# Optimization experiments

Measured on AMD Instinct MI355X. Metric: run time of the kernel, lower is better.

The kernel has to match this reference:

```python
import jax, jax.numpy as jnp
import numpy as np

B, S, D, H, W = 8, 2048, 128, 8, 64
INT_HEADS = 8          # hardcoded in SpatioTemporalLayer1
EPS_COS = 1e-8
EPS_LN = 1e-5


def _mha(q_in, k_in, v_in, in_w, in_b, out_w, out_b, nh, mask=None):
    # q_in/k_in/v_in: (batch, len, d); torch nn.MultiheadAttention math (eval, no dropout)
    b, lq, d = q_in.shape
    hd = d // nh
    q = (q_in @ in_w[:d].T + in_b[:d]).reshape(b, lq, nh, hd)
    k = (k_in @ in_w[d:2 * d].T + in_b[d:2 * d]).reshape(b, k_in.shape[1], nh, hd)
    v = (v_in @ in_w[2 * d:].T + in_b[2 * d:]).reshape(b, v_in.shape[1], nh, hd)
    scores = jnp.einsum('bihd,bjhd->bhij', q, k) / jnp.sqrt(jnp.asarray(hd, q_in.dtype))
    if mask is not None:
        scores = scores + mask
    attn = jax.nn.softmax(scores, axis=-1)
    out = jnp.einsum('bhij,bjhd->bihd', attn, v).reshape(b, lq, d)
    return out @ out_w.T + out_b


def _layernorm(x, g, b):
    mu = x.mean(-1, keepdims=True)
    var = ((x - mu) ** 2).mean(-1, keepdims=True)
    return (x - mu) * jax.lax.rsqrt(var + EPS_LN) * g + b


def _cos_normalize(e):
    n = jnp.maximum(jnp.linalg.norm(e, axis=-1, keepdims=True), EPS_COS)
    return e / n


def _forward(x, spatial_info, temporal_info,
             lw_in_w, lw_in_b, lw_out_w, lw_out_b,
             spat_w, spat_b, temp_w, temp_b,
             int_in_w, int_in_b, int_out_w, int_out_b,
             ffn_w1, ffn_b1, ffn_w2, ffn_b2,
             ln1_g, ln1_b, ln2_g, ln2_b):
    b, s, d = x.shape
    # --- local window attention (S % W == 0 here, so no padding path) ---
    nw = s // W
    xw = x.reshape(b * nw, W, d)
    causal = jnp.triu(jnp.full((W, W), -jnp.inf, x.dtype), k=1)
    attn = _mha(xw, xw, xw, lw_in_w, lw_in_b, lw_out_w, lw_out_b, H, causal).reshape(b, s, d)
    x = _layernorm(attn + x, ln1_g, ln1_b)
    # --- FFN (torch nn.GELU default = exact erf) ---
    h = jax.nn.gelu(x @ ffn_w1.T + ffn_b1, approximate=False)
    x = _layernorm(h @ ffn_w2.T + ffn_b2 + x, ln2_g, ln2_b)
    # --- spatio-temporal interaction ---
    se = spatial_info @ spat_w.T + spat_b
    te = temporal_info @ temp_w.T + temp_b
    sn = _cos_normalize(se)
    tn = _cos_normalize(te)
    ss = jnp.einsum('bid,bjd->bij', sn, sn)   # (B,S,S) spatial cosine sim
    ts = jnp.einsum('bid,bjd->bij', tn, tn)   # (B,S,S) temporal cosine sim
    # interaction MHA is batch_first=False: it treats (B,S,D) as (len=B, batch=S, d).
    # Equivalent batch-first call on swapped axes (faithful to the torch source).
    inter = jnp.swapaxes(
        _mha(jnp.swapaxes(se, 0, 1), jnp.swapaxes(te, 0, 1), jnp.swapaxes(te, 0, 1),
             int_in_w, int_in_b, int_out_w, int_out_b, INT_HEADS), 0, 1)
    # similarity[b,i,j,d] = ss[b,i,j]*ts[b,i,j]*inter[b,i,d]; mean over j factorizes:
    sim = (ss * ts).mean(axis=2)              # (B,S)
    return x + sim[..., None] * inter


def setup_inputs() -> dict:
    key = jax.random.key(0)
    ks = jax.random.split(key, 24)
    sc = 0.02
    inp = {
        'x': jax.random.normal(ks[0], (B, S, D), jnp.float32),
        'spatial_info': jax.random.normal(ks[1], (B, S, D), jnp.float32),
        'temporal_info': jax.random.normal(ks[2], (B, S, D), jnp.float32),
        'lw_in_w': jax.random.normal(ks[3], (3 * D, D), jnp.float32) * sc,
        'lw_in_b': jnp.zeros((3 * D,), jnp.float32),
        'lw_out_w': jax.random.normal(ks[4], (D, D), jnp.float32) * sc,
        'lw_out_b': jnp.zeros((D,), jnp.float32),
        'spat_w': jax.random.normal(ks[5], (D, D), jnp.float32) * sc,
        'spat_b': jnp.zeros((D,), jnp.float32),
        'temp_w': jax.random.normal(ks[6], (D, D), jnp.float32) * sc,
        'temp_b': jnp.zeros((D,), jnp.float32),
        'int_in_w': jax.random.normal(ks[7], (3 * D, D), jnp.float32) * sc,
        'int_in_b': jnp.zeros((3 * D,), jnp.float32),
        'int_out_w': jax.random.normal(ks[8], (D, D), jnp.float32) * sc,
        'int_out_b': jnp.zeros((D,), jnp.float32),
        'ffn_w1': jax.random.normal(ks[9], (4 * D, D), jnp.float32) * sc,
        'ffn_b1': jnp.zeros((4 * D,), jnp.float32),
        'ffn_w2': jax.random.normal(ks[10], (D, 4 * D), jnp.float32) * sc,
        'ffn_b2': jnp.zeros((D,), jnp.float32),
        'ln1_g': jnp.ones((D,), jnp.float32),
        'ln1_b': jnp.zeros((D,), jnp.float32),
        'ln2_g': jnp.ones((D,), jnp.float32),
        'ln2_b': jnp.zeros((D,), jnp.float32),
    }
    return inp


def reference(x, spatial_info, temporal_info,
              lw_in_w, lw_in_b, lw_out_w, lw_out_b,
              spat_w, spat_b, temp_w, temp_b,
              int_in_w, int_in_b, int_out_w, int_out_b,
              ffn_w1, ffn_b1, ffn_w2, ffn_b2,
              ln1_g, ln1_b, ln2_g, ln2_b):
    return _forward(x, spatial_info, temporal_info,
                    lw_in_w, lw_in_b, lw_out_w, lw_out_b,
                    spat_w, spat_b, temp_w, temp_b,
                    int_in_w, int_in_b, int_out_w, int_out_b,
                    ffn_w1, ffn_b1, ffn_w2, ffn_b2,
                    ln1_g, ln1_b, ln2_g, ln2_b)
```

## Files before the change

### kernel.cpp

```cpp
#include <hip/hip_runtime.h>
#include <math.h>

#define BB 8
#define SS 2048
#define NTOK (BB * SS)

using bf16x8 = __attribute__((ext_vector_type(8))) short;
using f32x4  = __attribute__((ext_vector_type(4))) float;

__device__ __forceinline__ float gelu_tanh(float x) {
    float y = 0.7978845608f * (x + 0.044715f * x * x * x);
    float e = __expf(2.0f * y);
    float t = 1.0f - 2.0f / (e + 1.0f);
    return 0.5f * x * (1.0f + t);
}
__device__ __forceinline__ unsigned short f2b(float f) {
    unsigned int u = __float_as_uint(f);
    u += 0x7FFFu + ((u >> 16) & 1u);
    return (unsigned short)(u >> 16);
}
__device__ __forceinline__ float b2f(unsigned short u) {
    return __uint_as_float((unsigned int)u << 16);
}
__device__ __forceinline__ bf16x8 ldg_f32_b8(const float* p) {
    float4 f0 = *(const float4*)p, f1 = *(const float4*)(p + 4);
    union { ushort4 u[2]; bf16x8 v; } r;
    r.u[0] = (ushort4){f2b(f0.x), f2b(f0.y), f2b(f0.z), f2b(f0.w)};
    r.u[1] = (ushort4){f2b(f1.x), f2b(f1.y), f2b(f1.z), f2b(f1.w)};
    return r.v;
}

__global__ __launch_bounds__(256) void phase1(
    const float* __restrict__ x,
    const float* __restrict__ lw_in_w, const float* __restrict__ b_in,
    const float* __restrict__ lw_out_w, const float* __restrict__ b_out,
    const float* __restrict__ lng, const float* __restrict__ lnb,
    float* __restrict__ x1, unsigned short* __restrict__ x1b,
    const float* __restrict__ ffn_w1, const float* __restrict__ ffn_w2,
    unsigned short* __restrict__ Wb,
    const float* __restrict__ int_in_w, const float* __restrict__ int_out_w,
    unsigned short* __restrict__ Wib, unsigned short* __restrict__ Wiob,
    float* __restrict__ Mf,
    const float* __restrict__ spatial, const float* __restrict__ temporal,
    const float* __restrict__ spat_w, const float* __restrict__ temp_w,
    const float* __restrict__ bsp, const float* __restrict__ btp,
    unsigned short* __restrict__ snb, unsigned short* __restrict__ tnb,
    unsigned short* __restrict__ seb, unsigned short* __restrict__ teb)
{
    __shared__ unsigned short Qs[64 * 136];
    __shared__ unsigned short Ks[64 * 136];
    __shared__ unsigned short Vt[128 * 72];
    __shared__ unsigned short Pb[4][32 * 72];
    __shared__ float red[2][64][2];
    const int tid = threadIdx.x;
    const int wv = tid >> 6, lane = tid & 63, ln = lane & 15, q = lane >> 4;

    if (blockIdx.x >= 320) {
        const int idx2 = blockIdx.x - 320;
        const int y = idx2 >> 8;
        const int m0 = (idx2 & 255) * 64;
        const float* Af = y ? temporal : spatial;
        const float* Wf = y ? temp_w : spat_w;
        const float* bias = y ? btp : bsp;
        unsigned short* nb = y ? tnb : snb;
        unsigned short* raw = y ? teb : seb;
        const int wm = (wv >> 1) * 32, wn = (wv & 1) * 64;

        f32x4 acc[2][4] = {};
        #pragma unroll
        for (int kf = 0; kf < 4; ++kf) {
            bf16x8 a[2], b[4];
            #pragma unroll
            for (int fm = 0; fm < 2; ++fm)
                a[fm] = ldg_f32_b8(Af + (size_t)(m0 + wm + fm * 16 + ln) * 128 + kf * 32 + q * 8);
            #pragma unroll
            for (int fn = 0; fn < 4; ++fn)
                b[fn] = ldg_f32_b8(Wf + (size_t)(wn + fn * 16 + ln) * 128 + kf * 32 + q * 8);
            #pragma unroll
            for (int fm = 0; fm < 2; ++fm)
                #pragma unroll
                for (int fn = 0; fn < 4; ++fn)
                    acc[fm][fn] = __builtin_amdgcn_mfma_f32_16x16x32_bf16(a[fm], b[fn], acc[fm][fn], 0, 0, 0);
        }
        #pragma unroll
        for (int fm = 0; fm < 2; ++fm)
            #pragma unroll
            for (int r = 0; r < 4; ++r) {
                int rl = wm + fm * 16 + q * 4 + r;
                float s2 = 0.0f;
                #pragma unroll
                for (int fn = 0; fn < 4; ++fn) {
                    int col = wn + fn * 16 + ln;
                    float vv = acc[fm][fn][r] + bias[col];
                    acc[fm][fn][r] = vv;
                    s2 += vv * vv;
                }
                #pragma unroll
                for (int off = 1; off < 16; off <<= 1) s2 += __shfl_xor(s2, off, 64);
                if (ln == 0) red[0][rl][wv & 1] = s2;
            }
        __syncthreads();
        #pragma unroll
        for (int fm = 0; fm < 2; ++fm)
            #pragma unroll
            for (int r = 0; r < 4; ++r) {
                int rl = wm + fm * 16 + q * 4 + r;
                int row = m0 + rl;
                float inv = 1.0f / fmaxf(sqrtf(red[0][rl][0] + red[0][rl][1]), 1e-8f);
                #pragma unroll
                for (int fn = 0; fn < 4; ++fn) {
                    int col = wn + fn * 16 + ln;
                    float vv = acc[fm][fn][r];
                    nb[(size_t)row * 128 + col] = f2b(vv * inv);
                    raw[(size_t)row * 128 + col] = f2b(vv);
                }
            }
        return;
    }

    if (blockIdx.x >= 256) {
        int gt = (blockIdx.x - 256) * 256 + tid;
        #pragma unroll
        for (int s = 0; s < 3; ++s) {
            int v = gt + s * 16384;
            const float* src;
            unsigned short* dst;
            int off;
            if (v < 16384)      { src = ffn_w1;   dst = Wb;         off = v; }
            else if (v < 32768) { src = ffn_w2;   dst = Wb + 65536; off = v - 16384; }
            else if (v < 45056) { src = int_in_w; dst = Wib;        off = v - 32768; }
            else                { src = int_out_w; dst = Wiob;      off = v - 45056; }
            float4 f = *(const float4*)(src + (size_t)off * 4);
            *(ushort4*)(dst + (size_t)off * 4) =
                (ushort4){f2b(f.x), f2b(f.y), f2b(f.z), f2b(f.w)};
        }
        float4 z4 = (float4){0.f, 0.f, 0.f, 0.f};
        *(float4*)(Mf + (size_t)gt * 4) = z4;
        *(float4*)(Mf + (size_t)(gt + 16384) * 4) = z4;
        return;
    }

    const int m0 = blockIdx.x * 64;
    const int wm = (wv >> 1) * 32, wn = (wv & 1) * 64;

    bf16x8 afr[4][2];
    #pragma unroll
    for (int kf = 0; kf < 4; ++kf)
        #pragma unroll
        for (int fm = 0; fm < 2; ++fm)
            afr[kf][fm] = ldg_f32_b8(x + (size_t)(m0 + wm + fm * 16 + ln) * 128 + kf * 32 + q * 8);

    #pragma unroll
    for (int p = 0; p < 3; ++p) {
        f32x4 acc[2][4] = {};
        #pragma unroll
        for (int kf = 0; kf < 4; ++kf) {
            bf16x8 b[4];
            #pragma unroll
            for (int fn = 0; fn < 4; ++fn)
                b[fn] = ldg_f32_b8(lw_in_w + (size_t)(p * 128 + wn + fn * 16 + ln) * 128 + kf * 32 + q * 8);
            #pragma unroll
            for (int fm = 0; fm < 2; ++fm)
                #pragma unroll
                for (int fn = 0; fn < 4; ++fn)
                    acc[fm][fn] = __builtin_amdgcn_mfma_f32_16x16x32_bf16(afr[kf][fm], b[fn], acc[fm][fn], 0, 0, 0);
        }
        #pragma unroll
        for (int fm = 0; fm < 2; ++fm)
            #pragma unroll
            for (int r = 0; r < 4; ++r) {
                int rl = wm + fm * 16 + q * 4 + r;
                #pragma unroll
                for (int fn = 0; fn < 4; ++fn) {
                    int col = wn + fn * 16 + ln;
                    unsigned short v = f2b(acc[fm][fn][r] + b_in[p * 128 + col]);
                    if (p == 0)      Qs[rl * 136 + col] = v;
                    else if (p == 1) Ks[rl * 136 + col] = v;
                    else             Vt[col * 72 + rl] = v;
                }
            }
    }
    __syncthreads();

    {
        const int mh = wv >> 1, hq = wv & 1;
        unsigned short* P = &Pb[wv][0];
        #pragma unroll
        for (int hh = 0; hh < 4; ++hh) {
            const int h = hq * 4 + hh;
            f32x4 sacc[2][4] = {};
            bf16x8 az[2] = {}, bz[4] = {};
            if (q < 2) {
                #pragma unroll
                for (int fm = 0; fm < 2; ++fm)
                    az[fm] = *(const bf16x8*)&Qs[(mh * 32 + fm * 16 + ln) * 136 + h * 16 + q * 8];
                #pragma unroll
                for (int fn = 0; fn < 4; ++fn)
                    bz[fn] = *(const bf16x8*)&Ks[(fn * 16 + ln) * 136 + h * 16 + q * 8];
            }
            #pragma unroll
            for (int fm = 0; fm < 2; ++fm)
                #pragma unroll
                for (int fn = 0; fn < 4; ++fn)
                    sacc[fm][fn] = __builtin_amdgcn_mfma_f32_16x16x32_bf16(az[fm], bz[fn], sacc[fm][fn], 0, 0, 0);
            float invr[2][4];
            #pragma unroll
            for (int fm = 0; fm < 2; ++fm)
                #pragma unroll
                for (int r = 0; r < 4; ++r) {
                    int gi = mh * 32 + fm * 16 + q * 4 + r;
                    float mx = -1e30f;
                    #pragma unroll
                    for (int fn = 0; fn < 4; ++fn) {
                        int j = fn * 16 + ln;
                        float s = sacc[fm][fn][r] * 0.25f;
                        if (j > gi) s = -1e30f;
                        sacc[fm][fn][r] = s;
                        mx = fmaxf(mx, s);
                    }
                    #pragma unroll
                    for (int off = 1; off < 16; off <<= 1)
                        mx = fmaxf(mx, __shfl_xor(mx, off, 64));
                    float sum = 0.0f;
                    #pragma unroll
                    for (int fn = 0; fn < 4; ++fn) {
                        float p_ = __expf(sacc[fm][fn][r] - mx);
                        sacc[fm][fn][r] = p_;
                        sum += p_;
                    }
                    #pragma unroll
                    for (int off = 1; off < 16; off <<= 1)
                        sum += __shfl_xor(sum, off, 64);
                    invr[fm][r] = 1.0f / sum;
                    #pragma unroll
                    for (int fn = 0; fn < 4; ++fn)
                        P[(fm * 16 + q * 4 + r) * 72 + fn * 16 + ln] = f2b(sacc[fm][fn][r]);
                }
            f32x4 oacc[2] = {};
            #pragma unroll
            for (int kf2 = 0; kf2 < 2; ++kf2) {
                bf16x8 pa[2], vb;
                #pragma unroll
                for (int fm = 0; fm < 2; ++fm)
                    pa[fm] = *(const bf16x8*)&P[(fm * 16 + ln) * 72 + kf2 * 32 + q * 8];
                vb = *(const bf16x8*)&Vt[(h * 16 + ln) * 72 + kf2 * 32 + q * 8];
                #pragma unroll
                for (int fm = 0; fm < 2; ++fm)
                    oacc[fm] = __builtin_amdgcn_mfma_f32_16x16x32_bf16(pa[fm], vb, oacc[fm], 0, 0, 0);
            }
            #pragma unroll
            for (int fm = 0; fm < 2; ++fm)
                #pragma unroll
                for (int r = 0; r < 4; ++r)
                    Qs[(mh * 32 + fm * 16 + q * 4 + r) * 136 + h * 16 + ln] =
                        f2b(oacc[fm][r] * invr[fm][r]);
        }
    }
    __syncthreads();

    f32x4 acc[2][4] = {};
    #pragma unroll
    for (int kf = 0; kf < 4; ++kf) {
        bf16x8 a[2], b[4];
        #pragma unroll
        for (int fm = 0; fm < 2; ++fm)
            a[fm] = *(const bf16x8*)&Qs[(wm + fm * 16 + ln) * 136 + kf * 32 + q * 8];
        #pragma unroll
        for (int fn = 0; fn < 4; ++fn)
            b[fn] = ldg_f32_b8(lw_out_w + (size_t)(wn + fn * 16 + ln) * 128 + kf * 32 + q * 8);
        #pragma unroll
        for (int fm = 0; fm < 2; ++fm)
            #pragma unroll
            for (int fn = 0; fn < 4; ++fn)
                acc[fm][fn] = __builtin_amdgcn_mfma_f32_16x16x32_bf16(a[fm], b[fn], acc[fm][fn], 0, 0, 0);
    }
    #pragma unroll
    for (int fm = 0; fm < 2; ++fm)
        #pragma unroll
        for (int r = 0; r < 4; ++r) {
            int rl = wm + fm * 16 + q * 4 + r;
            int row = m0 + rl;
            float s1 = 0.0f, s2 = 0.0f;
            #pragma unroll
            for (int fn = 0; fn < 4; ++fn) {
                int col = wn + fn * 16 + ln;
                float vv = acc[fm][fn][r] + b_out[col] + x[(size_t)row * 128 + col];
                acc[fm][fn][r] = vv;
                s1 += vv; s2 += vv * vv;
            }
            #pragma unroll
            for (int off = 1; off < 16; off <<= 1) {
                s1 += __shfl_xor(s1, off, 64);
                s2 += __shfl_xor(s2, off, 64);
            }
            if (ln == 0) { red[0][rl][wv & 1] = s1; red[1][rl][wv & 1] = s2; }
        }
    __syncthreads();
    #pragma unroll
    for (int fm = 0; fm < 2; ++fm)
        #pragma unroll
        for (int r = 0; r < 4; ++r) {
            int rl = wm + fm * 16 + q * 4 + r;
            int row = m0 + rl;
            float mu = (red[0][rl][0] + red[0][rl][1]) * (1.0f / 128.0f);
            float var = (red[1][rl][0] + red[1][rl][1]) * (1.0f / 128.0f) - mu * mu;
            float rs = rsqrtf(var + 1e-5f);
            #pragma unroll
            for (int fn = 0; fn < 4; ++fn) {
                int col = wn + fn * 16 + ln;
                float o = (acc[fm][fn][r] - mu) * rs * lng[col] + lnb[col];
                x1[(size_t)row * 128 + col] = o;
                x1b[(size_t)row * 128 + col] = f2b(o);
            }
        }
}

__global__ __launch_bounds__(256) void phase2(
    const unsigned short* __restrict__ x1b, const float* __restrict__ x1,
    const unsigned short* __restrict__ Wb,
    const float* __restrict__ b1, const float* __restrict__ b2,
    const float* __restrict__ lng, const float* __restrict__ lnb,
    float* __restrict__ x2,
    const unsigned short* __restrict__ snb, const unsigned short* __restrict__ tnb,
    float* __restrict__ Mf)
{
    __shared__ __align__(16) char pool[36864];
    __shared__ float red[2][64][2];
    const int tid = threadIdx.x;
    const int wv = tid >> 6, lane = tid & 63, ln = lane & 15, q = lane >> 4;

    if (blockIdx.x < 256) {
        unsigned short* Xs = (unsigned short*)pool;
        unsigned short* Hs0 = (unsigned short*)(pool + 17408);
        unsigned short* Hs1 = (unsigned short*)(pool + 26624);
        const int t0 = blockIdx.x * 64;
        const int wm = (wv >> 1) * 32;
        const int wn1 = (wv & 1) * 32, wn2 = (wv & 1) * 64;
        const unsigned short* w1 = Wb;
        const unsigned short* w2 = Wb + 65536;

        const uint4* X4 = (const uint4*)(x1b + (size_t)t0 * 128);
        #pragma unroll
        for (int t = 0; t < 4; ++t) {
            int idx = tid + t * 256;
            int r = idx >> 4, c = idx & 15;
            *(uint4*)&Xs[r * 136 + c * 8] = X4[r * 16 + c];
        }
        __syncthreads();

        f32x4 acc2[2][4] = {};
        for (int ch = 0; ch < 8; ++ch) {
            const int hc0 = ch * 64;
            unsigned short* Hb = (ch & 1) ? Hs1 : Hs0;
            f32x4 acc1[2][2] = {};
            #pragma unroll
            for (int kf = 0; kf < 4; ++kf) {
                bf16x8 a[2], b[2];
                #pragma unroll
                for (int fm = 0; fm < 2; ++fm)
                    a[fm] = *(const bf16x8*)&Xs[(wm + fm * 16 + ln) * 136 + kf * 32 + q * 8];
                #pragma unroll
                for (int fn = 0; fn < 2; ++fn)
                    b[fn] = *(const bf16x8*)&w1[(size_t)(hc0 + wn1 + fn * 16 + ln) * 128 + kf * 32 + q * 8];
                #pragma unroll
                for (int fm = 0; fm < 2; ++fm)
                    #pragma unroll
                    for (int fn = 0; fn < 2; ++fn)
                        acc1[fm][fn] = __builtin_amdgcn_mfma_f32_16x16x32_bf16(a[fm], b[fn], acc1[fm][fn], 0, 0, 0);
            }
            #pragma unroll
            for (int fm = 0; fm < 2; ++fm)
                #pragma unroll
                for (int fn = 0; fn < 2; ++fn)
                    #pragma unroll
                    for (int r = 0; r < 4; ++r) {
                        int rl = wm + fm * 16 + q * 4 + r;
                        int col = wn1 + fn * 16 + ln;
                        Hb[rl * 72 + col] = f2b(gelu_tanh(acc1[fm][fn][r] + b1[hc0 + col]));
                    }
            __syncthreads();
            #pragma unroll
            for (int kf2 = 0; kf2 < 2; ++kf2) {
                bf16x8 a[2], b[4];
                #pragma unroll
                for (int fm = 0; fm < 2; ++fm)
                    a[fm] = *(const bf16x8*)&Hb[(wm + fm * 16 + ln) * 72 + kf2 * 32 + q * 8];
                #pragma unroll
                for (int fn = 0; fn < 4; ++fn)
                    b[fn] = *(const bf16x8*)&w2[(size_t)(wn2 + fn * 16 + ln) * 512 + hc0 + kf2 * 32 + q * 8];
                #pragma unroll
                for (int fm = 0; fm < 2; ++fm)
                    #pragma unroll
                    for (int fn = 0; fn < 4; ++fn)
                        acc2[fm][fn] = __builtin_amdgcn_mfma_f32_16x16x32_bf16(a[fm], b[fn], acc2[fm][fn], 0, 0, 0);
            }
        }
        #pragma unroll
        for (int fm = 0; fm < 2; ++fm)
            #pragma unroll
            for (int r = 0; r < 4; ++r) {
                int rl = wm + fm * 16 + q * 4 + r;
                int row = t0 + rl;
                float s1 = 0.0f, s2 = 0.0f;
                #pragma unroll
                for (int fn = 0; fn < 4; ++fn) {
                    int col = wn2 + fn * 16 + ln;
                    float vv = acc2[fm][fn][r] + b2[col] + x1[(size_t)row * 128 + col];
                    acc2[fm][fn][r] = vv;
                    s1 += vv; s2 += vv * vv;
                }
                #pragma unroll
                for (int off = 1; off < 16; off <<= 1) {
                    s1 += __shfl_xor(s1, off, 64);
                    s2 += __shfl_xor(s2, off, 64);
                }
                if (ln == 0) { red[0][rl][wv & 1] = s1; red[1][rl][wv & 1] = s2; }
            }
        __syncthreads();
        #pragma unroll
        for (int fm = 0; fm < 2; ++fm)
            #pragma unroll
            for (int r = 0; r < 4; ++r) {
                int rl = wm + fm * 16 + q * 4 + r;
                int row = t0 + rl;
                float mu = (red[0][rl][0] + red[0][rl][1]) * (1.0f / 128.0f);
                float var = (red[1][rl][0] + red[1][rl][1]) * (1.0f / 128.0f) - mu * mu;
                float rs = rsqrtf(var + 1e-5f);
                #pragma unroll
                for (int fn = 0; fn < 4; ++fn) {
                    int col = wn2 + fn * 16 + ln;
                    x2[(size_t)row * 128 + col] = (acc2[fm][fn][r] - mu) * rs * lng[col] + lnb[col];
                }
            }
        return;
    }

    {
        unsigned short* Sst = (unsigned short*)pool;
        unsigned short* Tst = (unsigned short*)(pool + 17408);
        const int idx2 = blockIdx.x - 256;
        const int d0 = (idx2 & 1) * 64, e0 = ((idx2 >> 1) & 1) * 64;
        const int z = idx2 >> 2;
        const int b = z >> 4, chunk = z & 15;
        const size_t rowb = (size_t)(b * SS + chunk * 128);

        #pragma unroll
        for (int it = 0; it < 4; ++it) {
            int j = (tid & 31) + it * 32;
            int c8 = (tid >> 5) * 8;
            uint4 sv = *(const uint4*)&snb[(rowb + j) * 128 + d0 + c8];
            uint4 tv = *(const uint4*)&tnb[(rowb + j) * 128 + e0 + c8];
            const unsigned short* sp = (const unsigned short*)&sv;
            const unsigned short* tp = (const unsigned short*)&tv;
            #pragma unroll
            for (int c = 0; c < 8; ++c) {
                Sst[(c8 + c) * 136 + j] = sp[c];
                Tst[(c8 + c) * 136 + j] = tp[c];
            }
        }
        __syncthreads();

        const int wm = (wv >> 1) * 32, wn = (wv & 1) * 32;
        f32x4 acc[2][2] = {};
        #pragma unroll
        for (int kf = 0; kf < 4; ++kf) {
            bf16x8 a[2], bb[2];
            #pragma unroll
            for (int fm = 0; fm < 2; ++fm)
                a[fm] = *(const bf16x8*)&Tst[(wm + fm * 16 + ln) * 136 + kf * 32 + q * 8];
            #pragma unroll
            for (int fn = 0; fn < 2; ++fn)
                bb[fn] = *(const bf16x8*)&Sst[(wn + fn * 16 + ln) * 136 + kf * 32 + q * 8];
            #pragma unroll
            for (int fm = 0; fm < 2; ++fm)
                #pragma unroll
                for (int fn = 0; fn < 2; ++fn)
                    acc[fm][fn] = __builtin_amdgcn_mfma_f32_16x16x32_bf16(a[fm], bb[fn], acc[fm][fn], 0, 0, 0);
        }
        float* pp = Mf + (size_t)b * 16384;
        #pragma unroll
        for (int fm = 0; fm < 2; ++fm)
            #pragma unroll
            for (int r = 0; r < 4; ++r) {
                int ee = e0 + wm + fm * 16 + q * 4 + r;
                #pragma unroll
                for (int fn = 0; fn < 2; ++fn) {
                    int dd = d0 + wn + fn * 16 + ln;
                    unsafeAtomicAdd(&pp[(size_t)ee * 128 + dd], acc[fm][fn][r]);
                }
            }
    }
}

__global__ __launch_bounds__(256) void simgemm_kernel(
    const unsigned short* __restrict__ snb, const unsigned short* __restrict__ tnb,
    const float* __restrict__ Mf, float* __restrict__ sim)
{
    __shared__ float red[64][2];
    const int tid = threadIdx.x, m0 = blockIdx.x * 64, b = m0 >> 11;
    const int wv = tid >> 6, lane = tid & 63, ln = lane & 15, q = lane >> 4;
    const int wm = (wv >> 1) * 32, wn = (wv & 1) * 64;

    f32x4 acc[2][4] = {};
    #pragma unroll
    for (int kf = 0; kf < 4; ++kf) {
        bf16x8 a[2], bb[4];
        #pragma unroll
        for (int fm = 0; fm < 2; ++fm)
            a[fm] = *(const bf16x8*)&snb[(size_t)(m0 + wm + fm * 16 + ln) * 128 + kf * 32 + q * 8];
        #pragma unroll
        for (int fn = 0; fn < 4; ++fn)
            bb[fn] = ldg_f32_b8(Mf + (size_t)b * 16384 + (size_t)(wn + fn * 16 + ln) * 128 + kf * 32 + q * 8);
        #pragma unroll
        for (int fm = 0; fm < 2; ++fm)
            #pragma unroll
            for (int fn = 0; fn < 4; ++fn)
                acc[fm][fn] = __builtin_amdgcn_mfma_f32_16x16x32_bf16(a[fm], bb[fn], acc[fm][fn], 0, 0, 0);
    }
    #pragma unroll
    for (int fm = 0; fm < 2; ++fm)
        #pragma unroll
        for (int r = 0; r < 4; ++r) {
            int rl = wm + fm * 16 + q * 4 + r;
            int row = m0 + rl;
            float s = 0.0f;
            #pragma unroll
            for (int fn = 0; fn < 4; ++fn) {
                int col = wn + fn * 16 + ln;
                s += acc[fm][fn][r] * b2f(tnb[(size_t)row * 128 + col]);
            }
            #pragma unroll
            for (int off = 1; off < 16; off <<= 1) s += __shfl_xor(s, off, 64);
            if (ln == 0) red[rl][wv & 1] = s;
        }
    __syncthreads();
    if (tid < 64) sim[m0 + tid] = (red[tid][0] + red[tid][1]) * (1.0f / (float)SS);
}

__global__ __launch_bounds__(256) void inter_block(
    const unsigned short* __restrict__ seb, const unsigned short* __restrict__ teb,
    const unsigned short* __restrict__ Wib,
    const float* __restrict__ b_int,
    const unsigned short* __restrict__ Wiob,
    const float* __restrict__ b_io,
    const float* __restrict__ sim, const float* __restrict__ x2,
    float* __restrict__ out)
{
    __shared__ unsigned short Qs[64 * 136];
    __shared__ unsigned short KVs[64 * 256];
    const int tid = threadIdx.x, s0 = blockIdx.x * 8;
    const int wv = tid >> 6, lane = tid & 63, ln = lane & 15, q = lane >> 4;
    const int wm = (wv >> 1) * 32, wn = (wv & 1) * 64;

    bf16x8 afr[4][2];
    #pragma unroll
    for (int kf = 0; kf < 4; ++kf)
        #pragma unroll
        for (int fm = 0; fm < 2; ++fm) {
            int rl = wm + fm * 16 + ln;
            size_t g = (size_t)(rl >> 3) * 2048 + s0 + (rl & 7);
            afr[kf][fm] = *(const bf16x8*)&seb[g * 128 + kf * 32 + q * 8];
        }

    #pragma unroll
    for (int p = 0; p < 3; ++p) {
        if (p == 1) {
            #pragma unroll
            for (int kf = 0; kf < 4; ++kf)
                #pragma unroll
                for (int fm = 0; fm < 2; ++fm) {
                    int rl = wm + fm * 16 + ln;
                    size_t g = (size_t)(rl >> 3) * 2048 + s0 + (rl & 7);
                    afr[kf][fm] = *(const bf16x8*)&teb[g * 128 + kf * 32 + q * 8];
                }
        }
        f32x4 acc[2][4] = {};
        #pragma unroll
        for (int kf = 0; kf < 4; ++kf) {
            bf16x8 b[4];
            #pragma unroll
            for (int fn = 0; fn < 4; ++fn)
                b[fn] = *(const bf16x8*)&Wib[(size_t)(p * 128 + wn + fn * 16 + ln) * 128 + kf * 32 + q * 8];
            #pragma unroll
            for (int fm = 0; fm < 2; ++fm)
                #pragma unroll
                for (int fn = 0; fn < 4; ++fn)
                    acc[fm][fn] = __builtin_amdgcn_mfma_f32_16x16x32_bf16(afr[kf][fm], b[fn], acc[fm][fn], 0, 0, 0);
        }
        #pragma unroll
        for (int fm = 0; fm < 2; ++fm)
            #pragma unroll
            for (int r = 0; r < 4; ++r) {
                int rl = wm + fm * 16 + q * 4 + r;
                #pragma unroll
                for (int fn = 0; fn < 4; ++fn) {
                    int col = wn + fn * 16 + ln;
                    unsigned short v = f2b(acc[fm][fn][r] + b_int[p * 128 + col]);
                    if (p == 0) Qs[rl * 136 + col] = v;
                    else        KVs[rl * 256 + (p - 1) * 128 + col] = v;
                }
            }
        __syncthreads();
    }

    #pragma unroll
    for (int tt = 0; tt < 2; ++tt) {
        int task = tid + tt * 256;
        int ss = task >> 6, h = (task >> 3) & 7, i = task & 7;
        int rq = i * 8 + ss;
        float qr[16];
        {
            uint4 q0 = *(const uint4*)&Qs[rq * 136 + h * 16];
            uint4 q1 = *(const uint4*)&Qs[rq * 136 + h * 16 + 8];
            const unsigned short* p0 = (const unsigned short*)&q0;
            const unsigned short* p1 = (const unsigned short*)&q1;
            #pragma unroll
            for (int c = 0; c < 8; ++c) { qr[c] = b2f(p0[c]); qr[8 + c] = b2f(p1[c]); }
        }
        float sc[8];
        #pragma unroll
        for (int j = 0; j < 8; ++j) {
            uint4 k0 = *(const uint4*)&KVs[(j * 8 + ss) * 256 + h * 16];
            uint4 k1 = *(const uint4*)&KVs[(j * 8 + ss) * 256 + h * 16 + 8];
            const unsigned short* kp0 = (const unsigned short*)&k0;
            const unsigned short* kp1 = (const unsigned short*)&k1;
            float s = 0.0f;
            #pragma unroll
            for (int c = 0; c < 8; ++c) {
                s = fmaf(qr[c], b2f(kp0[c]), s);
                s = fmaf(qr[8 + c], b2f(kp1[c]), s);
            }
            sc[j] = s * 0.25f;
        }
        float mx = -1e30f;
        #pragma unroll
        for (int j = 0; j < 8; ++j) mx = fmaxf(mx, sc[j]);
        float pe[8], se = 0.0f;
        #pragma unroll
        for (int j = 0; j < 8; ++j) { pe[j] = __expf(sc[j] - mx); se += pe[j]; }
        float inv = 1.0f / se;
        float o[16] = {};
        #pragma unroll
        for (int j = 0; j < 8; ++j) {
            uint4 v0 = *(const uint4*)&KVs[(j * 8 + ss) * 256 + 128 + h * 16];
            uint4 v1 = *(const uint4*)&KVs[(j * 8 + ss) * 256 + 128 + h * 16 + 8];
            const unsigned short* vp0 = (const unsigned short*)&v0;
            const unsigned short* vp1 = (const unsigned short*)&v1;
            #pragma unroll
            for (int c = 0; c < 8; ++c) {
                o[c]     += pe[j] * b2f(vp0[c]);
                o[8 + c] += pe[j] * b2f(vp1[c]);
            }
        }
        ushort4 w0 = (ushort4){f2b(o[0]*inv),  f2b(o[1]*inv),  f2b(o[2]*inv),  f2b(o[3]*inv)};
        ushort4 w1 = (ushort4){f2b(o[4]*inv),  f2b(o[5]*inv),  f2b(o[6]*inv),  f2b(o[7]*inv)};
        ushort4 w2 = (ushort4){f2b(o[8]*inv),  f2b(o[9]*inv),  f2b(o[10]*inv), f2b(o[11]*inv)};
        ushort4 w3 = (ushort4){f2b(o[12]*inv), f2b(o[13]*inv), f2b(o[14]*inv), f2b(o[15]*inv)};
        *(ushort4*)&Qs[rq * 136 + h * 16]      = w0;
        *(ushort4*)&Qs[rq * 136 + h * 16 + 4]  = w1;
        *(ushort4*)&Qs[rq * 136 + h * 16 + 8]  = w2;
        *(ushort4*)&Qs[rq * 136 + h * 16 + 12] = w3;
    }
    __syncthreads();

    f32x4 acc[2][4] = {};
    #pragma unroll
    for (int kf = 0; kf < 4; ++kf) {
        bf16x8 a[2], b[4];
        #pragma unroll
        for (int fm = 0; fm < 2; ++fm)
            a[fm] = *(const bf16x8*)&Qs[(wm + fm * 16 + ln) * 136 + kf * 32 + q * 8];
        #pragma unroll
        for (int fn = 0; fn < 4; ++fn)
            b[fn] = *(const bf16x8*)&Wiob[(size_t)(wn + fn * 16 + ln) * 128 + kf * 32 + q * 8];
        #pragma unroll
        for (int fm = 0; fm < 2; ++fm)
            #pragma unroll
            for (int fn = 0; fn < 4; ++fn)
                acc[fm][fn] = __builtin_amdgcn_mfma_f32_16x16x32_bf16(a[fm], b[fn], acc[fm][fn], 0, 0, 0);
    }
    #pragma unroll
    for (int fm = 0; fm < 2; ++fm)
        #pragma unroll
        for (int r = 0; r < 4; ++r) {
            int rl = wm + fm * 16 + q * 4 + r;
            size_t g = (size_t)(rl >> 3) * 2048 + s0 + (rl & 7);
            float sc = sim[g];
            #pragma unroll
            for (int fn = 0; fn < 4; ++fn) {
                int col = wn + fn * 16 + ln;
                out[g * 128 + col] = (acc[fm][fn][r] + b_io[col]) * sc + x2[g * 128 + col];
            }
        }
}

extern "C" void kernel_launch(void* const* d_in, const int* in_sizes, int n_in,
                              void* d_out, int out_size, void* d_ws, size_t ws_size,
                              hipStream_t stream)
{
    const float* x        = (const float*)d_in[0];
    const float* spatial  = (const float*)d_in[1];
    const float* temporal = (const float*)d_in[2];
    const float* lw_in_w  = (const float*)d_in[3];
    const float* lw_in_b  = (const float*)d_in[4];
    const float* lw_out_w = (const float*)d_in[5];
    const float* lw_out_b = (const float*)d_in[6];
    const float* spat_w   = (const float*)d_in[7];
    const float* spat_b   = (const float*)d_in[8];
    const float* temp_w   = (const float*)d_in[9];
    const float* temp_b   = (const float*)d_in[10];
    const float* int_in_w = (const float*)d_in[11];
    const float* int_in_b = (const float*)d_in[12];
    const float* int_out_w= (const float*)d_in[13];
    const float* int_out_b= (const float*)d_in[14];
    const float* ffn_b1   = (const float*)d_in[16];
    const float* ffn_b2   = (const float*)d_in[18];
    const float* ln1_g    = (const float*)d_in[19];
    const float* ln1_b    = (const float*)d_in[20];
    const float* ln2_g    = (const float*)d_in[21];
    const float* ln2_b    = (const float*)d_in[22];
    float* out = (float*)d_out;

    char* base = (char*)d_ws;
    float*          x1   = (float*)(base + 0);
    unsigned short* x1b  = (unsigned short*)(base + 8388608);
    float*          x2   = (float*)(base + 12582912);
    unsigned short* snb  = (unsigned short*)(base + 20971520);
    unsigned short* tnb  = (unsigned short*)(base + 25165824);
    unsigned short* seb  = (unsigned short*)(base + 29360128);
    unsigned short* teb  = (unsigned short*)(base + 33554432);
    unsigned short* Wb   = (unsigned short*)(base + 37748736);
    unsigned short* Wib  = (unsigned short*)(base + 38010880);
    unsigned short* Wiob = (unsigned short*)(base + 38109184);
    float*          Mf   = (float*)(base + 38141952);
    float*          simb = (float*)(base + 38666240);

    phase1<<<832, 256, 0, stream>>>(
        x, lw_in_w, lw_in_b, lw_out_w, lw_out_b, ln1_g, ln1_b, x1, x1b,
        (const float*)d_in[15], (const float*)d_in[17], Wb,
        int_in_w, int_out_w, Wib, Wiob, Mf,
        spatial, temporal, spat_w, temp_w, spat_b, temp_b,
        snb, tnb, seb, teb);
    phase2<<<768, 256, 0, stream>>>(
        x1b, x1, Wb, ffn_b1, ffn_b2, ln2_g, ln2_b, x2, snb, tnb, Mf);
    simgemm_kernel<<<256, 256, 0, stream>>>(snb, tnb, Mf, simb);
    inter_block<<<256, 256, 0, stream>>>(
        seb, teb, Wib, int_in_b, Wiob, int_out_b, simb, x2, out);
}
```

Before: 219.1 us.

## Pre-convert all weights to bf16 in a separate kernel and restructure FFN per-wave

Adds a phase0 kernel that converts every weight matrix (including the local-attention and spatial/temporal projection weights) to bf16 once and zeroes Mf, so phase1 loads bf16 weight fragments directly instead of converting fp32 weights in every block. Phase2's FFN is restructured so each wave owns 16 full rows, keeps its A fragments in registers, stages GELU output in a per-wave LDS tile without block barriers, and does the LayerNorm reduction with shuffles only. The cost is an extra kernel launch and a serial dependency before phase1, plus each wave now reading the full W1/W2 slices.

```diff
diff --git a/kernel.cpp b/kernel.cpp
--- a/kernel.cpp
+++ b/kernel.cpp
@@ -30,19 +30,45 @@
     return r.v;
 }
 
+__global__ __launch_bounds__(256) void phase0(
+    const float* __restrict__ lw_in_w, const float* __restrict__ lw_out_w,
+    const float* __restrict__ spat_w, const float* __restrict__ temp_w,
+    const float* __restrict__ ffn_w1, const float* __restrict__ ffn_w2,
+    const float* __restrict__ int_in_w, const float* __restrict__ int_out_w,
+    unsigned short* __restrict__ Wlwb, unsigned short* __restrict__ Wstb,
+    unsigned short* __restrict__ Wb,
+    unsigned short* __restrict__ Wib, unsigned short* __restrict__ Wiob,
+    float* __restrict__ Mf)
+{
+    int v = blockIdx.x * 256 + threadIdx.x;
+    if (v < 73728) {
+        const float* src; unsigned short* dst; int off;
+        if (v < 12288)      { src = lw_in_w;   dst = Wlwb;          off = v; }
+        else if (v < 16384) { src = lw_out_w;  dst = Wlwb + 49152;  off = v - 12288; }
+        else if (v < 20480) { src = spat_w;    dst = Wstb;          off = v - 16384; }
+        else if (v < 24576) { src = temp_w;    dst = Wstb + 16384;  off = v - 20480; }
+        else if (v < 40960) { src = ffn_w1;    dst = Wb;            off = v - 24576; }
+        else if (v < 57344) { src = ffn_w2;    dst = Wb + 65536;    off = v - 40960; }
+        else if (v < 69632) { src = int_in_w;  dst = Wib;           off = v - 57344; }
+        else                { src = int_out_w; dst = Wiob;          off = v - 69632; }
+        float4 f = *(const float4*)(src + (size_t)off * 4);
+        *(ushort4*)(dst + (size_t)off * 4) =
+            (ushort4){f2b(f.x), f2b(f.y), f2b(f.z), f2b(f.w)};
+    } else {
+        *(float4*)(Mf + (size_t)(v - 73728) * 4) = (float4){0.f, 0.f, 0.f, 0.f};
+    }
+}
+
 __global__ __launch_bounds__(256) void phase1(
     const float* __restrict__ x,
-    const float* __restrict__ lw_in_w, const float* __restrict__ b_in,
-    const float* __restrict__ lw_out_w, const float* __restrict__ b_out,
+    const unsigned short* __restrict__ lwinb,
+    const float* __restrict__ b_in,
+    const unsigned short* __restrict__ lwoutb,
+    const float* __restrict__ b_out,
     const float* __restrict__ lng, const float* __restrict__ lnb,
     float* __restrict__ x1, unsigned short* __restrict__ x1b,
-    const float* __restrict__ ffn_w1, const float* __restrict__ ffn_w2,
-    unsigned short* __restrict__ Wb,
-    const float* __restrict__ int_in_w, const float* __restrict__ int_out_w,
-    unsigned short* __restrict__ Wib, unsigned short* __restrict__ Wiob,
-    float* __restrict__ Mf,
     const float* __restrict__ spatial, const float* __restrict__ temporal,
-    const float* __restrict__ spat_w, const float* __restrict__ temp_w,
+    const unsigned short* __restrict__ spwb, const unsigned short* __restrict__ tpwb,
     const float* __restrict__ bsp, const float* __restrict__ btp,
     unsigned short* __restrict__ snb, unsigned short* __restrict__ tnb,
     unsigned short* __restrict__ seb, unsigned short* __restrict__ teb)
@@ -55,12 +81,12 @@
     const int tid = threadIdx.x;
     const int wv = tid >> 6, lane = tid & 63, ln = lane & 15, q = lane >> 4;
 
-    if (blockIdx.x >= 320) {
-        const int idx2 = blockIdx.x - 320;
+    if (blockIdx.x >= 256) {
+        const int idx2 = blockIdx.x - 256;
         const int y = idx2 >> 8;
         const int m0 = (idx2 & 255) * 64;
         const float* Af = y ? temporal : spatial;
-        const float* Wf = y ? temp_w : spat_w;
+        const unsigned short* Wfb = y ? tpwb : spwb;
         const float* bias = y ? btp : bsp;
         unsigned short* nb = y ? tnb : snb;
         unsigned short* raw = y ? teb : seb;
@@ -75,7 +101,7 @@
                 a[fm] = ldg_f32_b8(Af + (size_t)(m0 + wm + fm * 16 + ln) * 128 + kf * 32 + q * 8);
             #pragma unroll
             for (int fn = 0; fn < 4; ++fn)
-                b[fn] = ldg_f32_b8(Wf + (size_t)(wn + fn * 16 + ln) * 128 + kf * 32 + q * 8);
+                b[fn] = *(const bf16x8*)&Wfb[(size_t)(wn + fn * 16 + ln) * 128 + kf * 32 + q * 8];
             #pragma unroll
             for (int fm = 0; fm < 2; ++fm)
                 #pragma unroll
@@ -118,28 +144,6 @@
         return;
     }
 
-    if (blockIdx.x >= 256) {
-        int gt = (blockIdx.x - 256) * 256 + tid;
-        #pragma unroll
-        for (int s = 0; s < 3; ++s) {
-            int v = gt + s * 16384;
-            const float* src;
-            unsigned short* dst;
-            int off;
-            if (v < 16384)      { src = ffn_w1;   dst = Wb;         off = v; }
-            else if (v < 32768) { src = ffn_w2;   dst = Wb + 65536; off = v - 16384; }
-            else if (v < 45056) { src = int_in_w; dst = Wib;        off = v - 32768; }
-            else                { src = int_out_w; dst = Wiob;      off = v - 45056; }
-            float4 f = *(const float4*)(src + (size_t)off * 4);
-            *(ushort4*)(dst + (size_t)off * 4) =
-                (ushort4){f2b(f.x), f2b(f.y), f2b(f.z), f2b(f.w)};
-        }
-        float4 z4 = (float4){0.f, 0.f, 0.f, 0.f};
-        *(float4*)(Mf + (size_t)gt * 4) = z4;
-        *(float4*)(Mf + (size_t)(gt + 16384) * 4) = z4;
-        return;
-    }
-
     const int m0 = blockIdx.x * 64;
     const int wm = (wv >> 1) * 32, wn = (wv & 1) * 64;
 
@@ -158,7 +162,7 @@
             bf16x8 b[4];
             #pragma unroll
             for (int fn = 0; fn < 4; ++fn)
-                b[fn] = ldg_f32_b8(lw_in_w + (size_t)(p * 128 + wn + fn * 16 + ln) * 128 + kf * 32 + q * 8);
+                b[fn] = *(const bf16x8*)&lwinb[(size_t)(p * 128 + wn + fn * 16 + ln) * 128 + kf * 32 + q * 8];
             #pragma unroll
             for (int fm = 0; fm < 2; ++fm)
                 #pragma unroll
@@ -267,7 +271,7 @@
             a[fm] = *(const bf16x8*)&Qs[(wm + fm * 16 + ln) * 136 + kf * 32 + q * 8];
         #pragma unroll
         for (int fn = 0; fn < 4; ++fn)
-            b[fn] = ldg_f32_b8(lw_out_w + (size_t)(wn + fn * 16 + ln) * 128 + kf * 32 + q * 8);
+            b[fn] = *(const bf16x8*)&lwoutb[(size_t)(wn + fn * 16 + ln) * 128 + kf * 32 + q * 8];
         #pragma unroll
         for (int fm = 0; fm < 2; ++fm)
             #pragma unroll
@@ -324,114 +328,79 @@
     const unsigned short* __restrict__ snb, const unsigned short* __restrict__ tnb,
     float* __restrict__ Mf)
 {
-    __shared__ __align__(16) char pool[36864];
-    __shared__ float red[2][64][2];
+    __shared__ __align__(16) char pool[34816];
     const int tid = threadIdx.x;
     const int wv = tid >> 6, lane = tid & 63, ln = lane & 15, q = lane >> 4;
 
     if (blockIdx.x < 256) {
-        unsigned short* Xs = (unsigned short*)pool;
-        unsigned short* Hs0 = (unsigned short*)(pool + 17408);
-        unsigned short* Hs1 = (unsigned short*)(pool + 26624);
+        unsigned short* Hw = (unsigned short*)pool + wv * 1152;
         const int t0 = blockIdx.x * 64;
-        const int wm = (wv >> 1) * 32;
-        const int wn1 = (wv & 1) * 32, wn2 = (wv & 1) * 64;
+        const int wm1 = wv * 16;
         const unsigned short* w1 = Wb;
         const unsigned short* w2 = Wb + 65536;
 
-        const uint4* X4 = (const uint4*)(x1b + (size_t)t0 * 128);
-        #pragma unroll
-        for (int t = 0; t < 4; ++t) {
-            int idx = tid + t * 256;
-            int r = idx >> 4, c = idx & 15;
-            *(uint4*)&Xs[r * 136 + c * 8] = X4[r * 16 + c];
-        }
-        __syncthreads();
-
-        f32x4 acc2[2][4] = {};
+        bf16x8 afr[4];
+        #pragma unroll
+        for (int kf = 0; kf < 4; ++kf)
+            afr[kf] = *(const bf16x8*)&x1b[(size_t)(t0 + wm1 + ln) * 128 + kf * 32 + q * 8];
+
+        f32x4 acc2[8] = {};
         for (int ch = 0; ch < 8; ++ch) {
             const int hc0 = ch * 64;
-            unsigned short* Hb = (ch & 1) ? Hs1 : Hs0;
-            f32x4 acc1[2][2] = {};
+            f32x4 acc1[4] = {};
             #pragma unroll
             for (int kf = 0; kf < 4; ++kf) {
-                bf16x8 a[2], b[2];
-                #pragma unroll
-                for (int fm = 0; fm < 2; ++fm)
-                    a[fm] = *(const bf16x8*)&Xs[(wm + fm * 16 + ln) * 136 + kf * 32 + q * 8];
-                #pragma unroll
-                for (int fn = 0; fn < 2; ++fn)
-                    b[fn] = *(const bf16x8*)&w1[(size_t)(hc0 + wn1 + fn * 16 + ln) * 128 + kf * 32 + q * 8];
-                #pragma unroll
-                for (int fm = 0; fm < 2; ++fm)
-                    #pragma unroll
-                    for (int fn = 0; fn < 2; ++fn)
-                        acc1[fm][fn] = __builtin_amdgcn_mfma_f32_16x16x32_bf16(a[fm], b[fn], acc1[fm][fn], 0, 0, 0);
-            }
-            #pragma unroll
-            for (int fm = 0; fm < 2; ++fm)
-                #pragma unroll
-                for (int fn = 0; fn < 2; ++fn)
-                    #pragma unroll
-                    for (int r = 0; r < 4; ++r) {
-                        int rl = wm + fm * 16 + q * 4 + r;
-                        int col = wn1 + fn * 16 + ln;
-                        Hb[rl * 72 + col] = f2b(gelu_tanh(acc1[fm][fn][r] + b1[hc0 + col]));
-                    }
-            __syncthreads();
+                bf16x8 b[4];
+                #pragma unroll
+                for (int fn = 0; fn < 4; ++fn)
+                    b[fn] = *(const bf16x8*)&w1[(size_t)(hc0 + fn * 16 + ln) * 128 + kf * 32 + q * 8];
+                #pragma unroll
+                for (int fn = 0; fn < 4; ++fn)
+                    acc1[fn] = __builtin_amdgcn_mfma_f32_16x16x32_bf16(afr[kf], b[fn], acc1[fn], 0, 0, 0);
+            }
+            #pragma unroll
+            for (int fn = 0; fn < 4; ++fn)
+                #pragma unroll
+                for (int r = 0; r < 4; ++r)
+                    Hw[(q * 4 + r) * 72 + fn * 16 + ln] =
+                        f2b(gelu_tanh(acc1[fn][r] + b1[hc0 + fn * 16 + ln]));
             #pragma unroll
             for (int kf2 = 0; kf2 < 2; ++kf2) {
-                bf16x8 a[2], b[4];
-                #pragma unroll
-                for (int fm = 0; fm < 2; ++fm)
-                    a[fm] = *(const bf16x8*)&Hb[(wm + fm * 16 + ln) * 72 + kf2 * 32 + q * 8];
-                #pragma unroll
-                for (int fn = 0; fn < 4; ++fn)
-                    b[fn] = *(const bf16x8*)&w2[(size_t)(wn2 + fn * 16 + ln) * 512 + hc0 + kf2 * 32 + q * 8];
-                #pragma unroll
-                for (int fm = 0; fm < 2; ++fm)
-                    #pragma unroll
-                    for (int fn = 0; fn < 4; ++fn)
-                        acc2[fm][fn] = __builtin_amdgcn_mfma_f32_16x16x32_bf16(a[fm], b[fn], acc2[fm][fn], 0, 0, 0);
-            }
-        }
-        #pragma unroll
-        for (int fm = 0; fm < 2; ++fm)
-            #pragma unroll
-            for (int r = 0; r < 4; ++r) {
-                int rl = wm + fm * 16 + q * 4 + r;
-                int row = t0 + rl;
-                float s1 = 0.0f, s2 = 0.0f;
-                #pragma unroll
-                for (int fn = 0; fn < 4; ++fn) {
-                    int col = wn2 + fn * 16 + ln;
-                    float vv = acc2[fm][fn][r] + b2[col] + x1[(size_t)row * 128 + col];
-                    acc2[fm][fn][r] = vv;
-                    s1 += vv; s2 += vv * vv;
-                }
-                #pragma unroll
-                for (int off = 1; off < 16; off <<= 1) {
-                    s1 += __shfl_xor(s1, off, 64);
-                    s2 += __shfl_xor(s2, off, 64);
-                }
-                if (ln == 0) { red[0][rl][wv & 1] = s1; red[1][rl][wv & 1] = s2; }
-            }
-        __syncthreads();
-        #pragma unroll
-        for (int fm = 0; fm < 2; ++fm)
-            #pragma unroll
-            for (int r = 0; r < 4; ++r) {
-                int rl = wm + fm * 16 + q * 4 + r;
-                int row = t0 + rl;
-                float mu = (red[0][rl][0] + red[0][rl][1]) * (1.0f / 128.0f);
-                float var = (red[1][rl][0] + red[1][rl][1]) * (1.0f / 128.0f) - mu * mu;
-                float rs = rsqrtf(var + 1e-5f);
-                #pragma unroll
-                for (int fn = 0; fn < 4; ++fn) {
-                    int col = wn2 + fn * 16 + ln;
-                    x2[(size_t)row * 128 + col] = (acc2[fm][fn][r] - mu) * rs * lng[col] + lnb[col];
-                }
-            }
+                bf16x8 a = *(const bf16x8*)&Hw[ln * 72 + kf2 * 32 + q * 8];
+                bf16x8 b8[8];
+                #pragma unroll
+                for (int fn = 0; fn < 8; ++fn)
+                    b8[fn] = *(const bf16x8*)&w2[(size_t)(fn * 16 + ln) * 512 + hc0 + kf2 * 32 + q * 8];
+                #pragma unroll
+                for (int fn = 0; fn < 8; ++fn)
+                    acc2[fn] = __builtin_amdgcn_mfma_f32_16x16x32_bf16(a, b8[fn], acc2[fn], 0, 0, 0);
+            }
+        }
+        #pragma unroll
+        for (int r = 0; r < 4; ++r) {
+            int row = t0 + wm1 + q * 4 + r;
+            float s1 = 0.0f, s2 = 0.0f;
+            #pragma unroll
+            for (int fn = 0; fn < 8; ++fn) {
+                int col = fn * 16 + ln;
+                float vv = acc2[fn][r] + b2[col] + x1[(size_t)row * 128 + col];
+                acc2[fn][r] = vv;
+                s1 += vv; s2 += vv * vv;
+            }
+            #pragma unroll
+            for (int off = 1; off < 16; off <<= 1) {
+                s1 += __shfl_xor(s1, off, 64);
+                s2 += __shfl_xor(s2, off, 64);
+            }
+            float mu = s1 * (1.0f / 128.0f);
+            float var = s2 * (1.0f / 128.0f) - mu * mu;
+            float rs = rsqrtf(var + 1e-5f);
+            #pragma unroll
+            for (int fn = 0; fn < 8; ++fn) {
+                int col = fn * 16 + ln;
+                x2[(size_t)row * 128 + col] = (acc2[fn][r] - mu) * rs * lng[col] + lnb[col];
+            }
+        }
         return;
     }
 
@@ -734,12 +703,16 @@
     unsigned short* Wiob = (unsigned short*)(base + 38109184);
     float*          Mf   = (float*)(base + 38141952);
     float*          simb = (float*)(base + 38666240);
-
-    phase1<<<832, 256, 0, stream>>>(
-        x, lw_in_w, lw_in_b, lw_out_w, lw_out_b, ln1_g, ln1_b, x1, x1b,
-        (const float*)d_in[15], (const float*)d_in[17], Wb,
-        int_in_w, int_out_w, Wib, Wiob, Mf,
-        spatial, temporal, spat_w, temp_w, spat_b, temp_b,
+    unsigned short* Wlwb = (unsigned short*)(base + 38731776);
+    unsigned short* Wstb = (unsigned short*)(base + 38862848);
+
+    phase0<<<416, 256, 0, stream>>>(
+        lw_in_w, lw_out_w, spat_w, temp_w,
+        (const float*)d_in[15], (const float*)d_in[17], int_in_w, int_out_w,
+        Wlwb, Wstb, Wb, Wib, Wiob, Mf);
+    phase1<<<768, 256, 0, stream>>>(
+        x, Wlwb, lw_in_b, Wlwb + 49152, lw_out_b, ln1_g, ln1_b, x1, x1b,
+        spatial, temporal, Wstb, Wstb + 16384, spat_b, temp_b,
         snb, tnb, seb, teb);
     phase2<<<768, 256, 0, stream>>>(
         x1b, x1, Wb, ffn_b1, ffn_b2, ln2_g, ln2_b, x2, snb, tnb, Mf);
```

Result: faster. 209.1 us (-4.6%).
